# Kernel optimization log

Measured on AMD Instinct MI355X. Metric: run time of the kernel, lower is better.

The kernel has to match this reference:

```python
import jax, jax.numpy as jnp
import numpy as np

B, L, D, H = 2, 4, 512, 8
HD = D // H
BLOCK, T_IDX, SEM = 2048, 2047, 50
NUM_VQ, CLIP = 1024, 512
T = T_IDX + 1  # condition token + idx tokens


def _ln(x, g, b):
    m = x.mean(-1, keepdims=True)
    v = ((x - m) ** 2).mean(-1, keepdims=True)
    return (x - m) * jax.lax.rsqrt(v + 1e-5) * g + b


def setup_inputs() -> dict:
    key = jax.random.key(0)
    ks = iter(jax.random.split(key, 48))
    p = lambda shape: 0.02 * jax.random.normal(next(ks), shape, jnp.float32)
    inp = {
        'idx': jax.random.randint(next(ks), (B, T_IDX), 0, NUM_VQ + 2, jnp.int32),
        'clip_feature': jax.random.normal(next(ks), (B, CLIP), jnp.float32),
        'tok_emb0': p((NUM_VQ + 2, D)),
        'tok_emb1': p((NUM_VQ + 2, D)),
        'cond_w': p((CLIP, D)), 'cond_b': jnp.zeros((D,), jnp.float32),
        'pos_emb': p((BLOCK, D)),
        'ln1_g': jnp.ones((L, D), jnp.float32), 'ln1_b': jnp.zeros((L, D), jnp.float32),
        'wq': p((L, D, D)), 'bq': jnp.zeros((L, D), jnp.float32),
        'wk': p((L, D, D)), 'bk': jnp.zeros((L, D), jnp.float32),
        'wv': p((L, D, D)), 'bv': jnp.zeros((L, D), jnp.float32),
        'wo': p((L, D, D)), 'bo': jnp.zeros((L, D), jnp.float32),
        'ln2_g': jnp.ones((L, D), jnp.float32), 'ln2_b': jnp.zeros((L, D), jnp.float32),
        'w1': p((L, D, 4 * D)), 'b1': jnp.zeros((L, 4 * D), jnp.float32),
        'w2': p((L, 4 * D, D)), 'b2': jnp.zeros((L, D), jnp.float32),
    }
    return inp


def reference(idx, clip_feature, tok_emb0, tok_emb1, cond_w, cond_b, pos_emb,
              ln1_g, ln1_b, wq, bq, wk, bk, wv, bv, wo, bo,
              ln2_g, ln2_b, w1, b1, w2, b2):
    # condition embedding + dual token embeddings (semantic / reconstruction split)
    cond = (clip_feature @ cond_w + cond_b)[:, None, :]          # [B,1,D]
    sem = tok_emb0[idx[:, :SEM]]                                  # [B,SEM,D]
    rec = tok_emb1[idx[:, SEM:]]                                  # [B,T_IDX-SEM,D]
    x = jnp.concatenate([cond, sem, rec], axis=1) + pos_emb[None, :T]  # [B,T,D]

    scale = 1.0 / np.sqrt(HD)
    causal = jnp.tril(jnp.ones((T, T), bool))                     # key <= query
    for i in range(L):
        h = _ln(x, ln1_g[i], ln1_b[i])
        q = (h @ wq[i] + bq[i]).reshape(B, T, H, HD)
        k = (h @ wk[i] + bk[i]).reshape(B, T, H, HD)
        v = (h @ wv[i] + bv[i]).reshape(B, T, H, HD)
        att = jnp.einsum('bthd,bshd->bhts', q, k) * scale        # [B,H,T,T]
        att = jnp.where(causal, att, -jnp.inf)
        att = jax.nn.softmax(att, axis=-1)
        y = jnp.einsum('bhts,bshd->bthd', att, v).reshape(B, T, D)
        x = x + y @ wo[i] + bo[i]
        h2 = _ln(x, ln2_g[i], ln2_b[i])
        x = x + jax.nn.gelu(h2 @ w1[i] + b1[i], approximate=False) @ w2[i] + b2[i]
    return x
```

## Files before the change

kernel.cpp:

```cpp
#include <hip/hip_runtime.h>
#include <math.h>

#define BB 2
#define TT 2048
#define DD 512
#define LL 4
#define HH 8
#define HDD 64
#define SEMN 50
#define CLIPN 512
#define NTOK (BB*TT)
#define QS 1024
#define VST 2056

typedef __bf16 bf16x8 __attribute__((ext_vector_type(8)));
typedef __bf16 bf16x4 __attribute__((ext_vector_type(4)));
typedef float  f32x4  __attribute__((ext_vector_type(4)));

#if __has_builtin(__builtin_amdgcn_global_load_lds)
#define USE_GLL 1
#endif

__device__ __forceinline__ void gll16(const __bf16* g, __bf16* l) {
#ifdef USE_GLL
  __builtin_amdgcn_global_load_lds((const __attribute__((address_space(1))) void*)g,
                                   (__attribute__((address_space(3))) void*)l, 16, 0, 0);
#endif
}

__device__ __forceinline__ float fexp2(float x) {
#if __has_builtin(__builtin_amdgcn_exp2f)
  return __builtin_amdgcn_exp2f(x);
#else
  return exp2f(x);
#endif
}

__global__ __launch_bounds__(128) void embed_kernel(
    const int* __restrict__ idx,
    const float* __restrict__ tok0, const float* __restrict__ tok1,
    const float* __restrict__ pos, float* __restrict__ x) {
  int row = blockIdx.x;
  int b = row / TT, t = row % TT;
  if (t == 0) return;
  int d4 = threadIdx.x << 2;
  int tok = idx[b*(TT-1) + (t-1)];
  const float* te = (t <= SEMN) ? tok0 : tok1;
  float4 e = *(const float4*)&te[(size_t)tok*DD + d4];
  float4 p = *(const float4*)&pos[(size_t)t*DD + d4];
  e.x += p.x; e.y += p.y; e.z += p.z; e.w += p.w;
  *(float4*)&x[(size_t)row*DD + d4] = e;
}

__global__ __launch_bounds__(256) void cond_kernel(
    const float* __restrict__ clip, const float* __restrict__ cw,
    const float* __restrict__ cb, const float* __restrict__ pos,
    float* __restrict__ x) {
  __shared__ float4 part[8][32];
  int b = blockIdx.x >> 2, dc = blockIdx.x & 3;
  int tid = threadIdx.x;
  int dv = tid & 31;
  int cg = tid >> 5;
  int d4 = dc*128 + dv*4;
  const float* cr = clip + b*CLIPN + cg*64;
  float4 acc = {0.f, 0.f, 0.f, 0.f};
  #pragma unroll 8
  for (int i = 0; i < 64; ++i) {
    float cv = cr[i];
    float4 w4 = *(const float4*)&cw[(size_t)(cg*64 + i)*DD + d4];
    acc.x = fmaf(cv, w4.x, acc.x); acc.y = fmaf(cv, w4.y, acc.y);
    acc.z = fmaf(cv, w4.z, acc.z); acc.w = fmaf(cv, w4.w, acc.w);
  }
  part[cg][dv] = acc;
  __syncthreads();
  if (tid < 32) {
    int dd4 = dc*128 + tid*4;
    float4 s = part[0][tid];
    #pragma unroll
    for (int g = 1; g < 8; ++g) {
      float4 q = part[g][tid];
      s.x += q.x; s.y += q.y; s.z += q.z; s.w += q.w;
    }
    float4 cbv = *(const float4*)&cb[dd4];
    float4 pv  = *(const float4*)&pos[dd4];
    s.x += cbv.x + pv.x; s.y += cbv.y + pv.y;
    s.z += cbv.z + pv.z; s.w += cbv.w + pv.w;
    *(float4*)&x[(size_t)(b*TT)*DD + dd4] = s;
  }
}

__global__ __launch_bounds__(256) void ln_kernel(const float* __restrict__ x,
                                                 const float* __restrict__ g,
                                                 const float* __restrict__ bta,
                                                 __bf16* __restrict__ out) {
  int l = threadIdx.x & 63;
  int row = blockIdx.x * 4 + (threadIdx.x >> 6);
  const float* xr = x + (size_t)row * DD + l*8;
  f32x4 a = *(const f32x4*)xr;
  f32x4 c = *(const f32x4*)(xr + 4);
  float s = a[0]+a[1]+a[2]+a[3]+c[0]+c[1]+c[2]+c[3];
  #pragma unroll
  for (int off = 1; off < 64; off <<= 1) s += __shfl_xor(s, off);
  float mean = s * (1.0f / DD);
  float d0 = a[0]-mean, d1 = a[1]-mean, d2 = a[2]-mean, d3 = a[3]-mean;
  float d4 = c[0]-mean, d5 = c[1]-mean, d6 = c[2]-mean, d7 = c[3]-mean;
  float sv = d0*d0+d1*d1+d2*d2+d3*d3+d4*d4+d5*d5+d6*d6+d7*d7;
  #pragma unroll
  for (int off = 1; off < 64; off <<= 1) sv += __shfl_xor(sv, off);
  float r = rsqrtf(sv * (1.0f / DD) + 1e-5f);
  f32x4 gv0 = *(const f32x4*)&g[l*8],   gv1 = *(const f32x4*)&g[l*8+4];
  f32x4 bv0 = *(const f32x4*)&bta[l*8], bv1 = *(const f32x4*)&bta[l*8+4];
  bf16x8 o;
  o[0] = (__bf16)(d0*r*gv0[0] + bv0[0]); o[1] = (__bf16)(d1*r*gv0[1] + bv0[1]);
  o[2] = (__bf16)(d2*r*gv0[2] + bv0[2]); o[3] = (__bf16)(d3*r*gv0[3] + bv0[3]);
  o[4] = (__bf16)(d4*r*gv1[0] + bv1[0]); o[5] = (__bf16)(d5*r*gv1[1] + bv1[1]);
  o[6] = (__bf16)(d6*r*gv1[2] + bv1[2]); o[7] = (__bf16)(d7*r*gv1[3] + bv1[3]);
  *(bf16x8*)&out[(size_t)row*DD + l*8] = o;
}

__global__ __launch_bounds__(256) void prep_kernel(
    const float* __restrict__ wq, const float* __restrict__ wk,
    const float* __restrict__ wv, const float* __restrict__ wo,
    const float* __restrict__ w1, const float* __restrict__ w2,
    __bf16* __restrict__ wbuf, size_t dstride) {
  __shared__ float tile[32][33];
  int id = blockIdx.x;
  int lay = blockIdx.y;
  size_t so4 = (size_t)lay * 262144, so16 = (size_t)lay * 1048576;
  __bf16* wb = wbuf + (size_t)lay * dstride;
  const float* src; __bf16* dst; int K, N, t;
  if (id < 1024) {
    int m = id >> 8; t = id & 255;
    src = ((m==0) ? wq : (m==1) ? wk : (m==2) ? wv : wo) + so4;
    dst = wb + (size_t)m * 262144; K = 512; N = 512;
  } else if (id < 2048) {
    t = id - 1024; src = w1 + so16; dst = wb + 1048576; K = 512; N = 2048;
  } else {
    t = id - 2048; src = w2 + so16; dst = wb + 2097152; K = 2048; N = 512;
  }
  int nsh = (N == 2048) ? 6 : 4;
  int tk = t >> nsh, tn = t & ((1 << nsh) - 1);
  int k0 = tk << 5, n0 = tn << 5;
  int tid = threadIdx.x;
  int r = tid >> 3, c = (tid & 7) << 2;
  float4 v = *(const float4*)&src[(size_t)(k0 + r)*N + n0 + c];
  tile[r][c+0] = v.x; tile[r][c+1] = v.y; tile[r][c+2] = v.z; tile[r][c+3] = v.w;
  __syncthreads();
  bf16x4 o;
  o[0] = (__bf16)tile[c+0][r];
  o[1] = (__bf16)tile[c+1][r];
  o[2] = (__bf16)tile[c+2][r];
  o[3] = (__bf16)tile[c+3][r];
  *(bf16x4*)&dst[(size_t)(n0 + r)*K + k0 + c] = o;
}

template<int TM, int TN, int QKV3, int RES, int GEL, int OB>
__global__ __launch_bounds__(256) void mgemm(
    const __bf16* __restrict__ A, const __bf16* __restrict__ Bt,
    const float* __restrict__ b0, const float* __restrict__ b1p, const float* __restrict__ b2p,
    const float* __restrict__ res, float* __restrict__ outF, __bf16* __restrict__ outB,
    __bf16* __restrict__ vtOut, int M, int N, int K, int ldo) {
  __shared__ __bf16 As[TM*64];
  __shared__ __bf16 Bs[TN*64];
  int tid = threadIdx.x, wave = tid >> 6, l = tid & 63;
  int l15 = l & 15, lg = l >> 4;
  int m0 = blockIdx.y * TM, n0 = blockIdx.x * TN;
  constexpr int WR = (TM == 128) ? 2 : 1;
  constexpr int WC = 4 / WR;
  constexpr int FM = TM / (16 * WR);
  constexpr int FN = TN / (16 * WC);
  int wr = wave / WC;
  int wc = wave % WC;

  f32x4 acc[FM][FN] = {};

  for (int k0 = 0; k0 < K; k0 += 64) {
#ifdef USE_GLL
    __syncthreads();
    #pragma unroll
    for (int g = wave; g < TM/8; g += 4) {
      int row = g*8 + (l >> 3);
      int lslot = (l & 7) ^ (row & 7);
      gll16(A + (size_t)(m0+row)*K + k0 + lslot*8, &As[g*512]);
    }
    #pragma unroll
    for (int g = wave; g < TN/8; g += 4) {
      int row = g*8 + (l >> 3);
      int lslot = (l & 7) ^ (row & 7);
      gll16(Bt + (size_t)(n0+row)*K + k0 + lslot*8, &Bs[g*512]);
    }
    asm volatile("s_waitcnt vmcnt(0)" ::: "memory");
    __syncthreads();
#else
    bf16x8 ar[TM/32], br[TN/32];
    #pragma unroll
    for (int c = 0; c < TM/32; ++c) {
      int idx = tid + c*256;
      int row = idx >> 3;
      int lslot = (idx & 7) ^ (row & 7);
      ar[c] = *(const bf16x8*)(A + (size_t)(m0+row)*K + k0 + lslot*8);
    }
    #pragma unroll
    for (int c = 0; c < TN/32; ++c) {
      int idx = tid + c*256;
      int row = idx >> 3;
      int lslot = (idx & 7) ^ (row & 7);
      br[c] = *(const bf16x8*)(Bt + (size_t)(n0+row)*K + k0 + lslot*8);
    }
    __syncthreads();
    #pragma unroll
    for (int c = 0; c < TM/32; ++c) {
      int idx = tid + c*256;
      *(bf16x8*)&As[(idx >> 3)*64 + (idx & 7)*8] = ar[c];
    }
    #pragma unroll
    for (int c = 0; c < TN/32; ++c) {
      int idx = tid + c*256;
      *(bf16x8*)&Bs[(idx >> 3)*64 + (idx & 7)*8] = br[c];
    }
    __syncthreads();
#endif
    bf16x8 af[FM][2], bfr[FN][2];
    #pragma unroll
    for (int mi = 0; mi < FM; ++mi) {
      int row = (wr*FM + mi)*16 + l15;
      #pragma unroll
      for (int h = 0; h < 2; ++h) {
        int ps = (h*4 + lg) ^ (row & 7);
        af[mi][h] = *(const bf16x8*)&As[row*64 + ps*8];
      }
    }
    #pragma unroll
    for (int ni = 0; ni < FN; ++ni) {
      int row = (wc*FN + ni)*16 + l15;
      #pragma unroll
      for (int h = 0; h < 2; ++h) {
        int ps = (h*4 + lg) ^ (row & 7);
        bfr[ni][h] = *(const bf16x8*)&Bs[row*64 + ps*8];
      }
    }
    #pragma unroll
    for (int mi = 0; mi < FM; ++mi)
      #pragma unroll
      for (int ni = 0; ni < FN; ++ni) {
        acc[mi][ni] = __builtin_amdgcn_mfma_f32_16x16x32_bf16(af[mi][0], bfr[ni][0], acc[mi][ni], 0, 0, 0);
        acc[mi][ni] = __builtin_amdgcn_mfma_f32_16x16x32_bf16(af[mi][1], bfr[ni][1], acc[mi][ni], 0, 0, 0);
      }
  }

  #pragma unroll
  for (int mi = 0; mi < FM; ++mi) {
    #pragma unroll
    for (int ni = 0; ni < FN; ++ni) {
      int col = n0 + (wc*FN + ni)*16 + l15;
      float bs;
      if (QKV3) bs = (col < 512) ? b0[col] : (col < 1024) ? b1p[col-512] : b2p[col-1024];
      else bs = b0[col];
      int row0 = m0 + (wr*FM + mi)*16 + (lg << 2);
      if (QKV3 && col >= 1024) {
        int hdg = col - 1024;
        bf16x4 pk;
        #pragma unroll
        for (int r = 0; r < 4; ++r) pk[r] = (__bf16)(acc[mi][ni][r] + bs);
        size_t vrow = (size_t)(((row0 >> 11)*8 + (hdg >> 6))*64 + (hdg & 63));
        *(bf16x4*)&vtOut[vrow*VST + (row0 & 2047)] = pk;
      } else {
        #pragma unroll
        for (int r = 0; r < 4; ++r) {
          int row = row0 + r;
          float v = acc[mi][ni][r] + bs;
          if (RES) v += res[(size_t)row*ldo + col];
          if (GEL) v = 0.5f * v * (1.0f + erff(v * 0.70710678118654752f));
          if (OB) outB[(size_t)row*ldo + col] = (__bf16)v;
          else    outF[(size_t)row*ldo + col] = v;
        }
      }
    }
  }
}

__global__ __launch_bounds__(256) void attn_kernel(const __bf16* __restrict__ qkv,
                                                   const __bf16* __restrict__ vt,
                                                   __bf16* __restrict__ y) {
  __shared__ float po[4][32][68];
  __shared__ float pmS[4][32];
  __shared__ float plS[4][4][32];
  int tid = threadIdx.x, wave = tid >> 6, l = tid & 63;
  int l15 = l & 15, lg = l >> 4;

  int wid = blockIdx.x;
  int g2 = 63 - (wid >> 4);
  int bh = wid & 15;
  int b = bh >> 3, h = bh & 7;
  int q0 = g2 * 32;

  const __bf16* qp = qkv + (size_t)(b*TT)*QS + h*HDD;
  const __bf16* kp = qp + 512;
  const __bf16* vtp = vt + ((size_t)bh*64 + l15)*VST + lg*8;
  const __bf16* kbase = kp + (size_t)l15*QS + lg*8;

  bf16x8 qf[2][2];
  {
    const float qs = 0.125f * 1.44269504088896f;
    #pragma unroll
    for (int f = 0; f < 2; ++f) {
      size_t qr = (size_t)(q0 + f*16 + l15) * QS + lg*8;
      bf16x8 t0 = *(const bf16x8*)(qp + qr);
      bf16x8 t1 = *(const bf16x8*)(qp + qr + 32);
      #pragma unroll
      for (int e = 0; e < 8; ++e) {
        qf[f][0][e] = (__bf16)((float)t0[e] * qs);
        qf[f][1][e] = (__bf16)((float)t1[e] * qs);
      }
    }
  }

  f32x4 o[2][4] = {};
  float m0 = 0.f, m1 = 0.f, ls0 = 0.f, ls1 = 0.f;
  int qpos0 = q0 + l15, qpos1 = q0 + 16 + l15;
  int nt = (q0 + 95) >> 6;
  int cs = (nt + 3) >> 2;
  int t0w = wave * cs;
  int t1w = t0w + cs; if (t1w > nt) t1w = nt;

  bf16x8 kA[4][2], kB[4][2], vv[8];

#define KLOAD(DST, KT) do {                                         \
    const __bf16* kr_ = kbase + (size_t)(KT)*64*QS;                 \
    _Pragma("unroll")                                               \
    for (int j_ = 0; j_ < 4; ++j_) {                                \
      DST[j_][0] = *(const bf16x8*)(kr_ + j_*16*QS);                \
      DST[j_][1] = *(const bf16x8*)(kr_ + j_*16*QS + 32);           \
    }                                                               \
  } while (0)

#define VLOAD(KT) do {                                              \
    const __bf16* vr_ = vtp + (KT)*64;                              \
    _Pragma("unroll")                                               \
    for (int hc_ = 0; hc_ < 4; ++hc_) {                             \
      vv[hc_]     = *(const bf16x8*)(vr_ + hc_*16*VST);             \
      vv[hc_ + 4] = *(const bf16x8*)(vr_ + hc_*16*VST + 32);        \
    }                                                               \
  } while (0)

#define PROCESS(KF, KT) do {                                                             \
    float sv[2][4][4];                                                                   \
    _Pragma("unroll")                                                                    \
    for (int f = 0; f < 2; ++f)                                                          \
      _Pragma("unroll")                                                                  \
      for (int j = 0; j < 4; ++j) {                                                      \
        f32x4 a_ = {};                                                                   \
        a_ = __builtin_amdgcn_mfma_f32_16x16x32_bf16(KF[j][0], qf[f][0], a_, 0, 0, 0);   \
        a_ = __builtin_amdgcn_mfma_f32_16x16x32_bf16(KF[j][1], qf[f][1], a_, 0, 0, 0);   \
        _Pragma("unroll")                                                                \
        for (int r = 0; r < 4; ++r) sv[f][j][r] = a_[r];                                 \
      }                                                                                  \
    if ((KT) == nt - 1) {                                                                \
      _Pragma("unroll")                                                                  \
      for (int j = 0; j < 4; ++j) {                                                      \
        int kb0 = (KT)*64 + j*16 + lg*4;                                                 \
        _Pragma("unroll")                                                                \
        for (int r = 0; r < 4; ++r) {                                                    \
          if (kb0 + r > qpos0) sv[0][j][r] = -1e30f;                                     \
          if (kb0 + r > qpos1) sv[1][j][r] = -1e30f;                                     \
        }                                                                                \
      }                                                                                  \
    }                                                                                    \
    float px0 = sv[0][0][0], px1 = sv[1][0][0];                                          \
    _Pragma("unroll")                                                                    \
    for (int j = 0; j < 4; ++j)                                                          \
      _Pragma("unroll")                                                                  \
      for (int r = 0; r < 4; ++r) {                                                      \
        px0 = fmaxf(px0, sv[0][j][r]);                                                   \
        px1 = fmaxf(px1, sv[1][j][r]);                                                   \
      }                                                                                  \
    if (!__all((px0 - m0 <= 8.0f) && (px1 - m1 <= 8.0f))) {                              \
      float u0 = px0, w0 = px0, u1 = px1, w1 = px1;                                      \
      asm("v_permlane32_swap_b32 %0, %1" : "+v"(u0), "+v"(w0));                          \
      float t0_ = fmaxf(u0, w0); u0 = t0_; w0 = t0_;                                     \
      asm("v_permlane16_swap_b32 %0, %1" : "+v"(u0), "+v"(w0));                          \
      float tm0 = fmaxf(u0, w0);                                                         \
      asm("v_permlane32_swap_b32 %0, %1" : "+v"(u1), "+v"(w1));                          \
      float t1_ = fmaxf(u1, w1); u1 = t1_; w1 = t1_;                                     \
      asm("v_permlane16_swap_b32 %0, %1" : "+v"(u1), "+v"(w1));                          \
      float tm1 = fmaxf(u1, w1);                                                         \
      float mn0 = fmaxf(m0, tm0), mn1 = fmaxf(m1, tm1);                                  \
      float fc0 = fexp2(m0 - mn0), fc1 = fexp2(m1 - mn1);                                \
      m0 = mn0; m1 = mn1;                                                                \
      ls0 *= fc0; ls1 *= fc1;                                                            \
      float a0_ = __shfl(fc0, lg*4+0), a1_ = __shfl(fc0, lg*4+1);                        \
      float a2_ = __shfl(fc0, lg*4+2), a3_ = __shfl(fc0, lg*4+3);                        \
      float b0_ = __shfl(fc1, lg*4+0), b1_ = __shfl(fc1, lg*4+1);                        \
      float b2_ = __shfl(fc1, lg*4+2), b3_ = __shfl(fc1, lg*4+3);                        \
      _Pragma("unroll")                                                                  \
      for (int hc = 0; hc < 4; ++hc) {                                                   \
        o[0][hc][0] *= a0_; o[0][hc][1] *= a1_; o[0][hc][2] *= a2_; o[0][hc][3] *= a3_;  \
        o[1][hc][0] *= b0_; o[1][hc][1] *= b1_; o[1][hc][2] *= b2_; o[1][hc][3] *= b3_;  \
      }                                                                                  \
    }                                                                                    \
    _Pragma("unroll")                                                                    \
    for (int f = 0; f < 2; ++f) {                                                        \
      float mm = f ? m1 : m0;                                                            \
      float p_[4][4];                                                                    \
      float rs_ = 0.f;                                                                   \
      _Pragma("unroll")                                                                  \
      for (int j = 0; j < 4; ++j)                                                        \
        _Pragma("unroll")                                                                \
        for (int r = 0; r < 4; ++r) { p_[j][r] = fexp2(sv[f][j][r] - mm); rs_ += p_[j][r]; } \
      if (f) ls1 += rs_; else ls0 += rs_;                                                \
      union PU { unsigned u[4]; bf16x8 v; };                                             \
      PU pa0, pa1;                                                                       \
      _Pragma("unroll")                                                                  \
      for (int pair = 0; pair < 2; ++pair) {                                             \
        unsigned c0, c1, d0, d1;                                                         \
        asm("v_cvt_pk_bf16_f32 %0, %1, %2" : "=v"(c0) : "v"(p_[2*pair][0]),   "v"(p_[2*pair][1]));   \
        asm("v_cvt_pk_bf16_f32 %0, %1, %2" : "=v"(c1) : "v"(p_[2*pair][2]),   "v"(p_[2*pair][3]));   \
        asm("v_cvt_pk_bf16_f32 %0, %1, %2" : "=v"(d0) : "v"(p_[2*pair+1][0]), "v"(p_[2*pair+1][1])); \
        asm("v_cvt_pk_bf16_f32 %0, %1, %2" : "=v"(d1) : "v"(p_[2*pair+1][2]), "v"(p_[2*pair+1][3])); \
        asm("v_permlane32_swap_b32 %0, %1" : "+v"(c0), "+v"(d0));                        \
        asm("v_permlane32_swap_b32 %0, %1" : "+v"(c1), "+v"(d1));                        \
        asm("v_permlane16_swap_b32 %0, %1" : "+v"(c0), "+v"(d0));                        \
        asm("v_permlane16_swap_b32 %0, %1" : "+v"(c1), "+v"(d1));                        \
        PU& pa = pair ? pa1 : pa0;                                                       \
        pa.u[0] = c0; pa.u[1] = c1; pa.u[2] = d0; pa.u[3] = d1;                          \
      }                                                                                  \
      _Pragma("unroll")                                                                  \
      for (int hc = 0; hc < 4; ++hc) {                                                   \
        o[f][hc] = __builtin_amdgcn_mfma_f32_16x16x32_bf16(pa0.v, vv[hc],     o[f][hc], 0, 0, 0); \
        o[f][hc] = __builtin_amdgcn_mfma_f32_16x16x32_bf16(pa1.v, vv[hc + 4], o[f][hc], 0, 0, 0); \
      }                                                                                  \
    }                                                                                    \
  } while (0)

  if (t0w < t1w) {
    KLOAD(kA, t0w);
    int kt = t0w;
    while (true) {
      VLOAD(kt);
      if (kt + 1 < t1w) KLOAD(kB, kt + 1);
      PROCESS(kA, kt);
      ++kt; if (kt >= t1w) break;
      VLOAD(kt);
      if (kt + 1 < t1w) KLOAD(kA, kt + 1);
      PROCESS(kB, kt);
      ++kt; if (kt >= t1w) break;
    }
  }

  #pragma unroll
  for (int f = 0; f < 2; ++f)
    #pragma unroll
    for (int hc = 0; hc < 4; ++hc)
      #pragma unroll
      for (int r = 0; r < 4; ++r)
        po[wave][f*16 + lg*4 + r][hc*16 + l15] = o[f][hc][r];
  plS[wave][lg][l15]      = ls0;
  plS[wave][lg][16 + l15] = ls1;
  if (l < 16) { pmS[wave][l] = m0; pmS[wave][16 + l] = m1; }
  __syncthreads();

  #pragma unroll
  for (int rep = 0; rep < 2; ++rep) {
    int q = wave*4 + lg + rep*16;
    float e0 = pmS[0][q], e1 = pmS[1][q], e2 = pmS[2][q], e3 = pmS[3][q];
    float mstar = fmaxf(fmaxf(e0, e1), fmaxf(e2, e3));
    float f0 = fexp2(e0 - mstar), f1 = fexp2(e1 - mstar);
    float f2 = fexp2(e2 - mstar), f3 = fexp2(e3 - mstar);
    float l0 = plS[0][0][q] + plS[0][1][q] + plS[0][2][q] + plS[0][3][q];
    float l1 = plS[1][0][q] + plS[1][1][q] + plS[1][2][q] + plS[1][3][q];
    float l2 = plS[2][0][q] + plS[2][1][q] + plS[2][2][q] + plS[2][3][q];
    float l3 = plS[3][0][q] + plS[3][1][q] + plS[3][2][q] + plS[3][3][q];
    float lstar = l0*f0 + l1*f1 + l2*f2 + l3*f3;
    float inv = 1.0f / lstar;
    f32x4 o0 = *(const f32x4*)&po[0][q][l15*4];
    f32x4 o1 = *(const f32x4*)&po[1][q][l15*4];
    f32x4 o2 = *(const f32x4*)&po[2][q][l15*4];
    f32x4 o3 = *(const f32x4*)&po[3][q][l15*4];
    bf16x4 outv;
    #pragma unroll
    for (int j = 0; j < 4; ++j)
      outv[j] = (__bf16)((o0[j]*f0 + o1[j]*f1 + o2[j]*f2 + o3[j]*f3) * inv);
    size_t base = (size_t)(b*TT + q0 + q) * DD + h*HDD + l15*4;
    *(bf16x4*)&y[base] = outv;
  }
}

extern "C" void kernel_launch(void* const* d_in, const int* in_sizes, int n_in,
                              void* d_out, int out_size, void* d_ws, size_t ws_size,
                              hipStream_t stream) {
  const int*   idx    = (const int*)d_in[0];
  const float* clip   = (const float*)d_in[1];
  const float* tok0   = (const float*)d_in[2];
  const float* tok1   = (const float*)d_in[3];
  const float* cond_w = (const float*)d_in[4];
  const float* cond_b = (const float*)d_in[5];
  const float* pos    = (const float*)d_in[6];
  const float* ln1_g  = (const float*)d_in[7];
  const float* ln1_b  = (const float*)d_in[8];
  const float* wq     = (const float*)d_in[9];
  const float* bq     = (const float*)d_in[10];
  const float* wk     = (const float*)d_in[11];
  const float* bk     = (const float*)d_in[12];
  const float* wv     = (const float*)d_in[13];
  const float* bv     = (const float*)d_in[14];
  const float* wo     = (const float*)d_in[15];
  const float* bo     = (const float*)d_in[16];
  const float* ln2_g  = (const float*)d_in[17];
  const float* ln2_b  = (const float*)d_in[18];
  const float* w1     = (const float*)d_in[19];
  const float* b1     = (const float*)d_in[20];
  const float* w2     = (const float*)d_in[21];
  const float* b2     = (const float*)d_in[22];

  float* x = (float*)d_out;
  char* wsb = (char*)d_ws;
  bool bigws = ws_size >= 46153728ULL;

  __bf16* wbuf; __bf16* h; __bf16* qkv; __bf16* yb; __bf16* vt; __bf16* ffn;
  size_t wstride;
  if (bigws) {
    wbuf = (__bf16*)wsb;
    wstride = 3145728;
    h    = (__bf16*)(wsb + 25165824);
    qkv  = (__bf16*)(wsb + 29360128);
    yb   = (__bf16*)(wsb + 37748736);
    vt   = (__bf16*)(wsb + 41943040);
    ffn  = qkv;
  } else {
    wbuf = (__bf16*)wsb;
    wstride = 0;
    h    = (__bf16*)(wsb + 6291456);
    qkv  = (__bf16*)(wsb + 10485760);
    yb   = (__bf16*)(wsb + 23068672);
    vt   = (__bf16*)(wsb + 27262976);
    ffn  = qkv;
  }

  embed_kernel<<<dim3(NTOK), 128, 0, stream>>>(idx, tok0, tok1, pos, x);
  cond_kernel<<<dim3(8), 256, 0, stream>>>(clip, cond_w, cond_b, pos, x);

  if (bigws)
    prep_kernel<<<dim3(3072, LL), 256, 0, stream>>>(wq, wk, wv, wo, w1, w2, wbuf, wstride);

  for (int i = 0; i < LL; ++i) {
    __bf16* wb = wbuf + (size_t)i * wstride;
    if (!bigws)
      prep_kernel<<<dim3(3072, 1), 256, 0, stream>>>(
          wq + (size_t)i*262144, wk + (size_t)i*262144, wv + (size_t)i*262144,
          wo + (size_t)i*262144, w1 + (size_t)i*1048576, w2 + (size_t)i*1048576, wb, 0);

    ln_kernel<<<NTOK/4, 256, 0, stream>>>(x, ln1_g + i*DD, ln1_b + i*DD, h);

    mgemm<64,128,1,0,0,1><<<dim3(12, 64), 256, 0, stream>>>(
        h, wb, bq + i*DD, bk + i*DD, bv + i*DD, nullptr, nullptr, qkv, vt, NTOK, 1536, 512, 1024);

    attn_kernel<<<dim3(1024), 256, 0, stream>>>(qkv, vt, yb);

    mgemm<64,64,0,1,0,0><<<dim3(8, 64), 256, 0, stream>>>(
        yb, wb + 786432, bo + i*DD, nullptr, nullptr, x, x, nullptr, nullptr, NTOK, 512, 512, 512);

    ln_kernel<<<NTOK/4, 256, 0, stream>>>(x, ln2_g + i*DD, ln2_b + i*DD, h);

    mgemm<128,128,0,0,1,1><<<dim3(16, 32), 256, 0, stream>>>(
        h, wb + 1048576, b1 + (size_t)i*4*DD, nullptr, nullptr, nullptr, nullptr, ffn, nullptr, NTOK, 4*DD, 512, 2048);

    mgemm<64,64,0,1,0,0><<<dim3(8, 64), 256, 0, stream>>>(
        ffn, wb + 2097152, b2 + i*DD, nullptr, nullptr, x, x, nullptr, nullptr, NTOK, 512, 2048, 512);
  }
}
```

Before: 447.9 us.

## Double-buffer LDS tiles in mgemm to overlap global loads with MFMA

Splits the shared A/B tiles into two buffers on the global_load_lds path. The next K-slice is staged asynchronously into the other buffer while MFMAs run on the current one, which leaves one barrier per iteration and aims to hide global memory latency. This doubles LDS use per block, which can lower occupancy. No explicit vmcnt wait comes before the in-loop barrier, so correctness relies on the barrier lowering waiting for the async LDS loads to finish.

```diff
diff --git a/kernel.cpp b/kernel.cpp
--- a/kernel.cpp
+++ b/kernel.cpp
@@ -160,8 +160,8 @@
     const float* __restrict__ b0, const float* __restrict__ b1p, const float* __restrict__ b2p,
     const float* __restrict__ res, float* __restrict__ outF, __bf16* __restrict__ outB,
     __bf16* __restrict__ vtOut, int M, int N, int K, int ldo) {
-  __shared__ __bf16 As[TM*64];
-  __shared__ __bf16 Bs[TN*64];
+  __shared__ __bf16 As[2][TM*64];
+  __shared__ __bf16 Bs[2][TN*64];
   int tid = threadIdx.x, wave = tid >> 6, l = tid & 63;
   int l15 = l & 15, lg = l >> 4;
   int m0 = blockIdx.y * TM, n0 = blockIdx.x * TN;
@@ -174,24 +174,61 @@
 
   f32x4 acc[FM][FN] = {};
 
-  for (int k0 = 0; k0 < K; k0 += 64) {
 #ifdef USE_GLL
-    __syncthreads();
+  auto stage = [&](int buf, int k0) {
     #pragma unroll
     for (int g = wave; g < TM/8; g += 4) {
       int row = g*8 + (l >> 3);
       int lslot = (l & 7) ^ (row & 7);
-      gll16(A + (size_t)(m0+row)*K + k0 + lslot*8, &As[g*512]);
+      gll16(A + (size_t)(m0+row)*K + k0 + lslot*8, &As[buf][g*512]);
     }
     #pragma unroll
     for (int g = wave; g < TN/8; g += 4) {
       int row = g*8 + (l >> 3);
       int lslot = (l & 7) ^ (row & 7);
-      gll16(Bt + (size_t)(n0+row)*K + k0 + lslot*8, &Bs[g*512]);
-    }
-    asm volatile("s_waitcnt vmcnt(0)" ::: "memory");
-    __syncthreads();
+      gll16(Bt + (size_t)(n0+row)*K + k0 + lslot*8, &Bs[buf][g*512]);
+    }
+  };
+  stage(0, 0);
+  asm volatile("s_waitcnt vmcnt(0)" ::: "memory");
+  __syncthreads();
+  int cur = 0;
+  for (int k0 = 0; k0 < K; k0 += 64) {
+    bool more = (k0 + 64 < K);
+    if (more) stage(cur ^ 1, k0 + 64);
+    const __bf16* Ac = As[cur];
+    const __bf16* Bc = Bs[cur];
+    bf16x8 af[FM][2], bfr[FN][2];
+    #pragma unroll
+    for (int mi = 0; mi < FM; ++mi) {
+      int row = (wr*FM + mi)*16 + l15;
+      #pragma unroll
+      for (int h = 0; h < 2; ++h) {
+        int ps = (h*4 + lg) ^ (row & 7);
+        af[mi][h] = *(const bf16x8*)&Ac[row*64 + ps*8];
+      }
+    }
+    #pragma unroll
+    for (int ni = 0; ni < FN; ++ni) {
+      int row = (wc*FN + ni)*16 + l15;
+      #pragma unroll
+      for (int h = 0; h < 2; ++h) {
+        int ps = (h*4 + lg) ^ (row & 7);
+        bfr[ni][h] = *(const bf16x8*)&Bc[row*64 + ps*8];
+      }
+    }
+    #pragma unroll
+    for (int mi = 0; mi < FM; ++mi)
+      #pragma unroll
+      for (int ni = 0; ni < FN; ++ni) {
+        acc[mi][ni] = __builtin_amdgcn_mfma_f32_16x16x32_bf16(af[mi][0], bfr[ni][0], acc[mi][ni], 0, 0, 0);
+        acc[mi][ni] = __builtin_amdgcn_mfma_f32_16x16x32_bf16(af[mi][1], bfr[ni][1], acc[mi][ni], 0, 0, 0);
+      }
+    if (more) __syncthreads();
+    cur ^= 1;
+  }
 #else
+  for (int k0 = 0; k0 < K; k0 += 64) {
     bf16x8 ar[TM/32], br[TN/32];
     #pragma unroll
     for (int c = 0; c < TM/32; ++c) {
@@ -211,15 +248,14 @@
     #pragma unroll
     for (int c = 0; c < TM/32; ++c) {
       int idx = tid + c*256;
-      *(bf16x8*)&As[(idx >> 3)*64 + (idx & 7)*8] = ar[c];
+      *(bf16x8*)&As[0][(idx >> 3)*64 + (idx & 7)*8] = ar[c];
     }
     #pragma unroll
     for (int c = 0; c < TN/32; ++c) {
       int idx = tid + c*256;
-      *(bf16x8*)&Bs[(idx >> 3)*64 + (idx & 7)*8] = br[c];
+      *(bf16x8*)&Bs[0][(idx >> 3)*64 + (idx & 7)*8] = br[c];
     }
     __syncthreads();
-#endif
     bf16x8 af[FM][2], bfr[FN][2];
     #pragma unroll
     for (int mi = 0; mi < FM; ++mi) {
@@ -227,7 +263,7 @@
       #pragma unroll
       for (int h = 0; h < 2; ++h) {
         int ps = (h*4 + lg) ^ (row & 7);
-        af[mi][h] = *(const bf16x8*)&As[row*64 + ps*8];
+        af[mi][h] = *(const bf16x8*)&As[0][row*64 + ps*8];
       }
     }
     #pragma unroll
@@ -236,7 +272,7 @@
       #pragma unroll
       for (int h = 0; h < 2; ++h) {
         int ps = (h*4 + lg) ^ (row & 7);
-        bfr[ni][h] = *(const bf16x8*)&Bs[row*64 + ps*8];
+        bfr[ni][h] = *(const bf16x8*)&Bs[0][row*64 + ps*8];
       }
     }
     #pragma unroll
@@ -247,6 +283,7 @@
         acc[mi][ni] = __builtin_amdgcn_mfma_f32_16x16x32_bf16(af[mi][1], bfr[ni][1], acc[mi][ni], 0, 0, 0);
       }
   }
+#endif
 
   #pragma unroll
   for (int mi = 0; mi < FM; ++mi) {
```

Measured after the change: 474.8 us. +6.0%, slower.
